# Kernel optimization log

Hardware: AMD Instinct MI355X
Metric: run time of the kernel (lower is better)

The kernel has to match this reference:

```python
import jax, jax.numpy as jnp
import numpy as np

N = 50000      # nodes
E = 800000     # edges (avg degree 16)
NFEAT = 256
NHID = 128
NCLASS = 40
NLAYERS_MID = 13  # gc2..gc14


def setup_inputs() -> dict:
    key = jax.random.key(0)
    ks = jax.random.split(key, 16)
    stdv_h = 1.0 / np.sqrt(NHID)     # GraphConvolution stdv = 1/sqrt(out_features)
    stdv_c = 1.0 / np.sqrt(NCLASS)
    u = lambda k, shape, s: jax.random.uniform(k, shape, jnp.float32, -s, s)
    return {
        "x": jax.random.normal(ks[0], (N, NFEAT), jnp.float32),
        "edge_src": jax.random.randint(ks[1], (E,), 0, N, jnp.int32),
        "edge_dst": jax.random.randint(ks[2], (E,), 0, N, jnp.int32),
        "edge_weight": jax.random.uniform(ks[3], (E,), jnp.float32),
        # skip-branch linear (self.weight / self.bias)
        "W0": u(ks[4], (NFEAT, NHID), stdv_h),
        "b0": u(ks[5], (NHID,), stdv_h),
        # gc1: nfeat -> nhid
        "W1": u(ks[6], (NFEAT, NHID), stdv_h),
        "b1": u(ks[7], (NHID,), stdv_h),
        # gc2..gc14: nhid -> nhid, stacked
        "Wmid": u(ks[8], (NLAYERS_MID, NHID, NHID), stdv_h),
        "bmid": u(ks[9], (NLAYERS_MID, NHID), stdv_h),
        # gc15: 14*nhid -> nclass
        "W15": u(ks[10], (14 * NHID, NCLASS), stdv_c),
        "b15": u(ks[11], (NCLASS,), stdv_c),
    }


def reference(x, edge_src, edge_dst, edge_weight, W0, b0, W1, b1, Wmid, bmid, W15, b15):
    n = x.shape[0]

    def gcn(h, W, b):
        # support = h @ W ; out = spmm(adj, support) + b  (adj as weighted edge list)
        support = h @ W
        msgs = support[edge_src] * edge_weight[:, None]           # [E, d]
        agg = jax.ops.segment_sum(msgs, edge_dst, num_segments=n)  # [N, d]
        return agg + b

    z = x @ W0 + b0
    x1 = jax.nn.relu(gcn(x, W1, b1)) + z

    def step(h, Wb):
        W, b = Wb
        hn = jax.nn.relu(gcn(h, W, b)) + h
        return hn, hn

    _, xs = jax.lax.scan(step, x1, (Wmid, bmid))   # xs: [13, N, NHID] = x2..x14
    all_x = jnp.concatenate([x1[None], xs], axis=0)  # [14, N, NHID] = x1..x14
    # concat order in torch code: (x14, x13, ..., x1)
    x_cat = jnp.swapaxes(all_x[::-1], 0, 1).reshape(n, 14 * NHID)
    # dropout is identity in eval mode
    x15 = gcn(x_cat, W15, b15)
    return jax.nn.log_softmax(x15, axis=1)
```

## Files before the change

kernel.cpp:

```cpp
#include <hip/hip_runtime.h>
#include <stdint.h>

#define NN 50000
#define EE 800000
#define DH 128
#define NC 40
#define KCAT (14*DH)
#define CAP 64

typedef __bf16 bf16x8 __attribute__((ext_vector_type(8)));
typedef float floatx4 __attribute__((ext_vector_type(4)));

__device__ __forceinline__ float bf2f(unsigned short u) {
  union { uint32_t i; float f; } v; v.i = ((uint32_t)u) << 16; return v.f;
}
__device__ __forceinline__ unsigned short f2bf(float f) {
  union { float f; uint32_t i; } v; v.f = f;
  uint32_t x = v.i;
  uint32_t r = (x + 0x7fffu + ((x >> 16) & 1u)) >> 16;
  return (unsigned short)r;
}

__global__ void init_counts_detect(int* counts, const unsigned short* xw) {
  int i = blockIdx.x * blockDim.x + threadIdx.x;
  if (i < NN) counts[i] = 0;
  if (blockIdx.x == 0) {
    int t = threadIdx.x;
    int wild = 0;
    for (int k = t; k < 4096; k += 256) {
      unsigned e = (xw[k] >> 7) & 0xFF;
      if (e >= 0x90) wild++;
    }
    __shared__ int red[256];
    red[t] = wild;
    __syncthreads();
    for (int s = 128; s > 0; s >>= 1) {
      if (t < s) red[t] += red[t + s];
      __syncthreads();
    }
    if (t == 0) counts[NN] = red[0];
  }
}

__global__ void convert_f4(const void* in, unsigned short* outp, int n4, const int* flag) {
  bool isf32 = (*flag) > 32;
  for (int i = blockIdx.x * blockDim.x + threadIdx.x; i < n4;
       i += gridDim.x * blockDim.x) {
    ushort4 o;
    if (isf32) {
      float4 v = ((const float4*)in)[i];
      o.x = f2bf(v.x); o.y = f2bf(v.y); o.z = f2bf(v.z); o.w = f2bf(v.w);
    } else {
      o = ((const ushort4*)in)[i];
    }
    ((ushort4*)outp)[i] = o;
  }
}

__global__ void convert_bias(const void* b0, const void* b1, const void* bm,
                             const void* b15, unsigned short* bb, const int* flag) {
  bool isf32 = (*flag) > 32;
  int i = blockIdx.x * blockDim.x + threadIdx.x;
  if (i >= 1960) return;
  const void* src; int off;
  if (i < 128)        { src = b0;  off = i; }
  else if (i < 256)   { src = b1;  off = i - 128; }
  else if (i < 1920)  { src = bm;  off = i - 256; }
  else                { src = b15; off = i - 1920; }
  bb[i] = isf32 ? f2bf(((const float*)src)[off]) : ((const unsigned short*)src)[off];
}

__global__ void transpose_w(const void* B, unsigned short* BT,
                            int L, int K, int M, int Mpad, const int* flag) {
  bool isf32 = (*flag) > 32;
  int total = L * Mpad * K;
  for (int idx = blockIdx.x * blockDim.x + threadIdx.x; idx < total;
       idx += gridDim.x * blockDim.x) {
    int k = idx % K;
    int n = (idx / K) % Mpad;
    int l = idx / (K * Mpad);
    unsigned short v = 0;
    if (n < M) {
      size_t si = (size_t)l * K * M + (size_t)k * M + n;
      v = isf32 ? f2bf(((const float*)B)[si]) : ((const unsigned short*)B)[si];
    }
    BT[idx] = v;
  }
}

__global__ void build_ell(const int* __restrict__ src, const int* __restrict__ dst,
                          const void* __restrict__ w,
                          int* __restrict__ cnt, int2* __restrict__ ell,
                          const int* __restrict__ flag) {
  bool isf32 = (*flag) > 32;
  int e = blockIdx.x * blockDim.x + threadIdx.x;
  if (e >= EE) return;
  int d = dst[e];
  if ((unsigned)d >= NN) return;
  int p = atomicAdd(&cnt[d], 1);
  if (p >= CAP) return;
  int s = src[e];
  float wf = isf32 ? ((const float*)w)[e] : bf2f(((const unsigned short*)w)[e]);
  if ((unsigned)s >= NN) { s = 0; wf = 0.f; }
  union { float f; int i; } wv; wv.f = wf;
  ell[(size_t)d * CAP + p] = make_int2(s, wv.i);
}

template <int K>
__global__ __launch_bounds__(256) void gemm_direct(
    const unsigned short* __restrict__ A, int lda,
    const unsigned short* __restrict__ BT,
    unsigned short* __restrict__ C, int ldc,
    const unsigned short* __restrict__ bias) {
  int t = threadIdx.x;
  int wave = t >> 6, lane = t & 63;
  int q = lane >> 4, mn = lane & 15;
  int r0 = blockIdx.x * 64;
  int wcol = wave * 32;

  const unsigned short* ap[4];
  #pragma unroll
  for (int i = 0; i < 4; ++i) {
    int r = r0 + i * 16 + mn;
    if (r >= NN) r = NN - 1;
    ap[i] = A + (size_t)r * lda + q * 8;
  }
  const unsigned short* bp[2];
  #pragma unroll
  for (int j = 0; j < 2; ++j) bp[j] = BT + (size_t)(wcol + j * 16 + mn) * K + q * 8;

  floatx4 acc[4][2];
  floatx4 zf = {0.f, 0.f, 0.f, 0.f};
  #pragma unroll
  for (int i = 0; i < 4; ++i)
    #pragma unroll
    for (int j = 0; j < 2; ++j) acc[i][j] = zf;

  #pragma unroll
  for (int kc = 0; kc < K; kc += 64) {
    bf16x8 fa[4][2], fb[2][2];
    #pragma unroll
    for (int i = 0; i < 4; ++i)
      #pragma unroll
      for (int ks = 0; ks < 2; ++ks)
        fa[i][ks] = *(const bf16x8*)(ap[i] + kc + ks * 32);
    #pragma unroll
    for (int j = 0; j < 2; ++j)
      #pragma unroll
      for (int ks = 0; ks < 2; ++ks)
        fb[j][ks] = *(const bf16x8*)(bp[j] + kc + ks * 32);
    #pragma unroll
    for (int ks = 0; ks < 2; ++ks)
      #pragma unroll
      for (int i = 0; i < 4; ++i)
        #pragma unroll
        for (int j = 0; j < 2; ++j)
          acc[i][j] = __builtin_amdgcn_mfma_f32_16x16x32_bf16(fa[i][ks], fb[j][ks],
                                                              acc[i][j], 0, 0, 0);
  }

  #pragma unroll
  for (int j = 0; j < 2; ++j) {
    int col = wcol + j * 16 + mn;
    float badd = bias ? bf2f(bias[col]) : 0.0f;
    #pragma unroll
    for (int i = 0; i < 4; ++i) {
      int rbase = r0 + i * 16 + q * 4;
      #pragma unroll
      for (int rr = 0; rr < 4; ++rr) {
        int row = rbase + rr;
        if (row < NN) C[(size_t)row * ldc + col] = f2bf(acc[i][j][rr] + badd);
      }
    }
  }
}

__global__ __launch_bounds__(256) void gemm_cat_direct(
    const unsigned short* __restrict__ A,
    const unsigned short* __restrict__ BT,
    float* __restrict__ C) {
  int t = threadIdx.x;
  int wave = t >> 6, lane = t & 63;
  int q = lane >> 4, mn = lane & 15;
  int r0 = blockIdx.x * 64 + wave * 16;
  int ar = r0 + mn;
  if (ar >= NN) ar = NN - 1;
  const unsigned short* ap = A + (size_t)ar * KCAT + q * 8;
  const unsigned short* bp[3];
  #pragma unroll
  for (int j = 0; j < 3; ++j) bp[j] = BT + (size_t)(j * 16 + mn) * KCAT + q * 8;

  floatx4 acc[3];
  floatx4 zf = {0.f, 0.f, 0.f, 0.f};
  #pragma unroll
  for (int j = 0; j < 3; ++j) acc[j] = zf;

  #pragma unroll 2
  for (int kc = 0; kc < KCAT; kc += 64) {
    bf16x8 fa[2], fb[3][2];
    #pragma unroll
    for (int ks = 0; ks < 2; ++ks) fa[ks] = *(const bf16x8*)(ap + kc + ks * 32);
    #pragma unroll
    for (int j = 0; j < 3; ++j)
      #pragma unroll
      for (int ks = 0; ks < 2; ++ks)
        fb[j][ks] = *(const bf16x8*)(bp[j] + kc + ks * 32);
    #pragma unroll
    for (int ks = 0; ks < 2; ++ks)
      #pragma unroll
      for (int j = 0; j < 3; ++j)
        acc[j] = __builtin_amdgcn_mfma_f32_16x16x32_bf16(fa[ks], fb[j][ks], acc[j],
                                                         0, 0, 0);
  }

  #pragma unroll
  for (int j = 0; j < 3; ++j) {
    int col = j * 16 + mn;
    if (col < NC) {
      #pragma unroll
      for (int rr = 0; rr < 4; ++rr) {
        int row = r0 + q * 4 + rr;
        if (row < NN) C[(size_t)row * NC + col] = acc[j][rr];
      }
    }
  }
}

__global__ __launch_bounds__(256) void spmm_layer(
    const unsigned short* __restrict__ support, const int* __restrict__ cnt,
    const int2* __restrict__ ell, const unsigned short* __restrict__ bias,
    const unsigned short* __restrict__ res, int res_stride,
    unsigned short* __restrict__ out, int out_stride) {
  int wave = threadIdx.x >> 6, lane = threadIdx.x & 63;
  int row = blockIdx.x * 4 + wave;
  if (row >= NN) return;
  int n = cnt[row];
  if (n > CAP) n = CAP;
  int2 ev = ell[(size_t)row * CAP + lane];
  float a0 = 0.f, a1 = 0.f;
  int j = 0;
  for (; j + 16 <= n; j += 16) {
    uint32_t g[16];
    int sidx[16];
    #pragma unroll
    for (int u = 0; u < 16; ++u) sidx[u] = __shfl(ev.x, j + u);
    #pragma unroll
    for (int u = 0; u < 16; ++u)
      g[u] = *(const uint32_t*)(support + (size_t)sidx[u] * DH + 2 * lane);
    #pragma unroll
    for (int u = 0; u < 16; ++u) {
      union { int i; float f; } wv; wv.i = __shfl(ev.y, j + u);
      a0 += wv.f * bf2f((unsigned short)(g[u] & 0xffff));
      a1 += wv.f * bf2f((unsigned short)(g[u] >> 16));
    }
  }
  for (; j + 8 <= n; j += 8) {
    uint32_t g[8];
    int sidx[8];
    #pragma unroll
    for (int u = 0; u < 8; ++u) sidx[u] = __shfl(ev.x, j + u);
    #pragma unroll
    for (int u = 0; u < 8; ++u)
      g[u] = *(const uint32_t*)(support + (size_t)sidx[u] * DH + 2 * lane);
    #pragma unroll
    for (int u = 0; u < 8; ++u) {
      union { int i; float f; } wv; wv.i = __shfl(ev.y, j + u);
      a0 += wv.f * bf2f((unsigned short)(g[u] & 0xffff));
      a1 += wv.f * bf2f((unsigned short)(g[u] >> 16));
    }
  }
  for (; j < n; ++j) {
    int s = __shfl(ev.x, j);
    union { int i; float f; } wv; wv.i = __shfl(ev.y, j);
    uint32_t g = *(const uint32_t*)(support + (size_t)s * DH + 2 * lane);
    a0 += wv.f * bf2f((unsigned short)(g & 0xffff));
    a1 += wv.f * bf2f((unsigned short)(g >> 16));
  }
  uint32_t bw = *(const uint32_t*)(bias + 2 * lane);
  uint32_t rw = *(const uint32_t*)(res + (size_t)row * res_stride + 2 * lane);
  float v0 = fmaxf(a0 + bf2f((unsigned short)(bw & 0xffff)), 0.f) +
             bf2f((unsigned short)(rw & 0xffff));
  float v1 = fmaxf(a1 + bf2f((unsigned short)(bw >> 16)), 0.f) +
             bf2f((unsigned short)(rw >> 16));
  uint32_t o = (uint32_t)f2bf(v0) | ((uint32_t)f2bf(v1) << 16);
  *(uint32_t*)(out + (size_t)row * out_stride + 2 * lane) = o;
}

__global__ __launch_bounds__(256) void spmm_softmax_out(
    const float* __restrict__ s15, const int* __restrict__ cnt,
    const int2* __restrict__ ell, const unsigned short* __restrict__ bias,
    float* __restrict__ out) {
  int wave = threadIdx.x >> 6, lane = threadIdx.x & 63;
  int row = blockIdx.x * 4 + wave;
  if (row >= NN) return;
  int n = cnt[row];
  if (n > CAP) n = CAP;
  int2 ev = ell[(size_t)row * CAP + lane];
  int fl = lane < NC ? lane : NC - 1;
  float acc = 0.f;
  int j = 0;
  for (; j + 4 <= n; j += 4) {
    float g[4];
    #pragma unroll
    for (int u = 0; u < 4; ++u) {
      int s = __shfl(ev.x, j + u);
      g[u] = s15[(size_t)s * NC + fl];
    }
    #pragma unroll
    for (int u = 0; u < 4; ++u) {
      union { int i; float f; } wv; wv.i = __shfl(ev.y, j + u);
      acc += wv.f * g[u];
    }
  }
  for (; j < n; ++j) {
    int s = __shfl(ev.x, j);
    union { int i; float f; } wv; wv.i = __shfl(ev.y, j);
    acc += wv.f * s15[(size_t)s * NC + fl];
  }
  acc += bf2f(bias[fl]);
  float v = (lane < NC) ? acc : -3.0e38f;
  float m = v;
  #pragma unroll
  for (int off = 32; off > 0; off >>= 1) m = fmaxf(m, __shfl_xor(m, off));
  float e = (lane < NC) ? expf(v - m) : 0.f;
  float sum = e;
  #pragma unroll
  for (int off = 32; off > 0; off >>= 1) sum += __shfl_xor(sum, off);
  if (lane < NC) out[(size_t)row * NC + lane] = v - m - logf(sum);
}

extern "C" void kernel_launch(void* const* d_in, const int* in_sizes, int n_in,
                              void* d_out, int out_size, void* d_ws, size_t ws_size,
                              hipStream_t stream) {
  const void* x   = d_in[0];
  const int* esrc = (const int*)d_in[1];
  const int* edst = (const int*)d_in[2];
  const void* ew  = d_in[3];
  const void* W0  = d_in[4];
  const void* b0  = d_in[5];
  const void* W1  = d_in[6];
  const void* b1  = d_in[7];
  const void* Wm  = d_in[8];
  const void* bm  = d_in[9];
  const void* W15 = d_in[10];
  const void* b15 = d_in[11];
  float* out = (float*)d_out;

  char* ws = (char*)d_ws;
  size_t off = 0;
  auto alloc = [&](size_t bytes) -> void* {
    void* p = ws + off;
    off = (off + bytes + 255) & ~(size_t)255;
    return p;
  };
  unsigned short* xcat = (unsigned short*)alloc((size_t)NN * KCAT * 2);
  unsigned short* xbf  = (unsigned short*)alloc((size_t)NN * 256 * 2);
  unsigned short* supp = (unsigned short*)alloc((size_t)NN * DH * 2);
  unsigned short* zbuf = (unsigned short*)alloc((size_t)NN * DH * 2);
  float* s15           = (float*)alloc((size_t)NN * NC * 4);
  int* counts          = (int*)alloc((size_t)(NN + 1) * 4);
  int2* ell            = (int2*)alloc((size_t)NN * CAP * 8);
  unsigned short* W0T  = (unsigned short*)alloc((size_t)256 * 128 * 2);
  unsigned short* W1T  = (unsigned short*)alloc((size_t)256 * 128 * 2);
  unsigned short* WmT  = (unsigned short*)alloc((size_t)13 * 128 * 128 * 2);
  unsigned short* W15T = (unsigned short*)alloc((size_t)48 * 1792 * 2);
  unsigned short* bb   = (unsigned short*)alloc((size_t)(128 + 128 + 13 * 128 + 40) * 2);
  if (off > ws_size) return;
  int* flag = counts + NN;
  unsigned short* b0b  = bb;
  unsigned short* b1b  = bb + 128;
  unsigned short* bmb  = bb + 256;
  unsigned short* b15b = bb + 256 + 13 * 128;

  init_counts_detect<<<197, 256, 0, stream>>>(counts, (const unsigned short*)x);
  transpose_w<<<128, 256, 0, stream>>>(W0, W0T, 1, 256, 128, 128, flag);
  transpose_w<<<128, 256, 0, stream>>>(W1, W1T, 1, 256, 128, 128, flag);
  transpose_w<<<832, 256, 0, stream>>>(Wm, WmT, 13, 128, 128, 128, flag);
  transpose_w<<<336, 256, 0, stream>>>(W15, W15T, 1, 1792, 40, 48, flag);
  convert_f4<<<2048, 256, 0, stream>>>(x, xbf, NN * 256 / 4, flag);
  convert_bias<<<8, 256, 0, stream>>>(b0, b1, bm, b15, bb, flag);
  build_ell<<<3125, 256, 0, stream>>>(esrc, edst, ew, counts, ell, flag);

  int gb = (NN + 63) / 64;
  int sb = (NN + 3) / 4;
  gemm_direct<256><<<gb, 256, 0, stream>>>(xbf, 256, W0T, zbuf, DH, b0b);
  gemm_direct<256><<<gb, 256, 0, stream>>>(xbf, 256, W1T, supp, DH, nullptr);
  spmm_layer<<<sb, 256, 0, stream>>>(supp, counts, ell, b1b, zbuf, DH,
                                     xcat + 13 * DH, KCAT);
  for (int l = 0; l < 13; ++l) {
    gemm_direct<128><<<gb, 256, 0, stream>>>(xcat + (13 - l) * DH, KCAT,
                                             WmT + l * 128 * 128, supp, DH, nullptr);
    spmm_layer<<<sb, 256, 0, stream>>>(supp, counts, ell, bmb + l * DH,
                                       xcat + (13 - l) * DH, KCAT,
                                       xcat + (12 - l) * DH, KCAT);
  }
  gemm_cat_direct<<<gb, 256, 0, stream>>>(xcat, W15T, s15);
  spmm_softmax_out<<<sb, 256, 0, stream>>>(s15, counts, ell, b15b, out);
}
```

Baseline: 1.093 ms.

## Stage GEMM A tiles in LDS via direct global-to-LDS loads and fuse first GEMMs

After: 1.017 ms. 6.9% less time.

```diff
diff --git a/kernel.cpp b/kernel.cpp
--- a/kernel.cpp
+++ b/kernel.cpp
@@ -10,6 +10,11 @@
 
 typedef __bf16 bf16x8 __attribute__((ext_vector_type(8)));
 typedef float floatx4 __attribute__((ext_vector_type(4)));
+
+#define GLOAD_LDS16(gp, lp)                                                          \
+  __builtin_amdgcn_global_load_lds(                                                  \
+      (const __attribute__((address_space(1))) uint32_t*)(gp),                       \
+      (__attribute__((address_space(3))) uint32_t*)(lp), 16, 0, 0)
 
 __device__ __forceinline__ float bf2f(unsigned short u) {
   union { uint32_t i; float f; } v; v.i = ((uint32_t)u) << 16; return v.f;
@@ -106,111 +111,183 @@
   ell[(size_t)d * CAP + p] = make_int2(s, wv.i);
 }
 
-template <int K>
-__global__ __launch_bounds__(256) void gemm_direct(
-    const unsigned short* __restrict__ A, int lda,
+__global__ __launch_bounds__(256) void gemm_first(
+    const unsigned short* __restrict__ A,
     const unsigned short* __restrict__ BT,
-    unsigned short* __restrict__ C, int ldc,
+    unsigned short* __restrict__ C0,
+    unsigned short* __restrict__ C1,
     const unsigned short* __restrict__ bias) {
+  __shared__ unsigned short As[64 * 256];
   int t = threadIdx.x;
   int wave = t >> 6, lane = t & 63;
   int q = lane >> 4, mn = lane & 15;
   int r0 = blockIdx.x * 64;
-  int wcol = wave * 32;
-
-  const unsigned short* ap[4];
-  #pragma unroll
-  for (int i = 0; i < 4; ++i) {
-    int r = r0 + i * 16 + mn;
-    if (r >= NN) r = NN - 1;
-    ap[i] = A + (size_t)r * lda + q * 8;
-  }
-  const unsigned short* bp[2];
-  #pragma unroll
-  for (int j = 0; j < 2; ++j) bp[j] = BT + (size_t)(wcol + j * 16 + mn) * K + q * 8;
-
-  floatx4 acc[4][2];
+
+  #pragma unroll
+  for (int cc = 0; cc < 8; ++cc) {
+    int L = cc * 4096 + t * 16;
+    int row = L >> 9;
+    int colb = (L & 511) ^ ((row & 7) << 4);
+    int gr = r0 + row; if (gr >= NN) gr = NN - 1;
+    GLOAD_LDS16((const char*)A + (size_t)gr * 512 + colb, (char*)As + L);
+  }
+  __syncthreads();
+
+  floatx4 acc[4][4];
   floatx4 zf = {0.f, 0.f, 0.f, 0.f};
   #pragma unroll
   for (int i = 0; i < 4; ++i)
     #pragma unroll
-    for (int j = 0; j < 2; ++j) acc[i][j] = zf;
-
-  #pragma unroll
-  for (int kc = 0; kc < K; kc += 64) {
-    bf16x8 fa[4][2], fb[2][2];
+    for (int j = 0; j < 4; ++j) acc[i][j] = zf;
+
+  #pragma unroll
+  for (int ks = 0; ks < 8; ++ks) {
+    bf16x8 fa[4], fb[4];
+    #pragma unroll
+    for (int i = 0; i < 4; ++i) {
+      int row = i * 16 + mn;
+      fa[i] = *(const bf16x8*)((const char*)As + row * 512 +
+                               ((ks * 64 + q * 16) ^ ((row & 7) << 4)));
+    }
+    #pragma unroll
+    for (int j = 0; j < 4; ++j)
+      fb[j] = *(const bf16x8*)((const char*)BT +
+                               (size_t)(wave * 64 + j * 16 + mn) * 512 + ks * 64 + q * 16);
     #pragma unroll
     for (int i = 0; i < 4; ++i)
       #pragma unroll
-      for (int ks = 0; ks < 2; ++ks)
-        fa[i][ks] = *(const bf16x8*)(ap[i] + kc + ks * 32);
-    #pragma unroll
-    for (int j = 0; j < 2; ++j)
-      #pragma unroll
-      for (int ks = 0; ks < 2; ++ks)
-        fb[j][ks] = *(const bf16x8*)(bp[j] + kc + ks * 32);
-    #pragma unroll
-    for (int ks = 0; ks < 2; ++ks)
-      #pragma unroll
-      for (int i = 0; i < 4; ++i)
-        #pragma unroll
-        for (int j = 0; j < 2; ++j)
-          acc[i][j] = __builtin_amdgcn_mfma_f32_16x16x32_bf16(fa[i][ks], fb[j][ks],
-                                                              acc[i][j], 0, 0, 0);
-  }
-
-  #pragma unroll
-  for (int j = 0; j < 2; ++j) {
-    int col = wcol + j * 16 + mn;
-    float badd = bias ? bf2f(bias[col]) : 0.0f;
+      for (int j = 0; j < 4; ++j)
+        acc[i][j] = __builtin_amdgcn_mfma_f32_16x16x32_bf16(fa[i], fb[j], acc[i][j], 0, 0, 0);
+  }
+
+  #pragma unroll
+  for (int j = 0; j < 4; ++j) {
+    int col = wave * 64 + j * 16 + mn;
+    bool is0 = col < 128;
+    int ccol = is0 ? col : col - 128;
+    unsigned short* Cp = is0 ? C0 : C1;
+    float badd = is0 ? bf2f(bias[ccol]) : 0.f;
     #pragma unroll
     for (int i = 0; i < 4; ++i) {
       int rbase = r0 + i * 16 + q * 4;
       #pragma unroll
       for (int rr = 0; rr < 4; ++rr) {
         int row = rbase + rr;
-        if (row < NN) C[(size_t)row * ldc + col] = f2bf(acc[i][j][rr] + badd);
+        if (row < NN) Cp[(size_t)row * 128 + ccol] = f2bf(acc[i][j][rr] + badd);
       }
     }
   }
 }
 
-__global__ __launch_bounds__(256) void gemm_cat_direct(
+__global__ __launch_bounds__(256) void gemm_mid(
+    const unsigned short* __restrict__ A,
+    const unsigned short* __restrict__ BT,
+    unsigned short* __restrict__ C) {
+  __shared__ unsigned short As[32 * 128];
+  int t = threadIdx.x;
+  int wave = t >> 6, lane = t & 63;
+  int q = lane >> 4, mn = lane & 15;
+  int r0 = blockIdx.x * 32;
+
+  #pragma unroll
+  for (int cc = 0; cc < 2; ++cc) {
+    int L = cc * 4096 + t * 16;
+    int row = L >> 8;
+    int colb = (L & 255) ^ ((row & 7) << 4);
+    int gr = r0 + row; if (gr >= NN) gr = NN - 1;
+    GLOAD_LDS16((const char*)A + (size_t)gr * (KCAT * 2) + colb, (char*)As + L);
+  }
+  __syncthreads();
+
+  floatx4 acc[2][2];
+  floatx4 zf = {0.f, 0.f, 0.f, 0.f};
+  #pragma unroll
+  for (int i = 0; i < 2; ++i)
+    #pragma unroll
+    for (int j = 0; j < 2; ++j) acc[i][j] = zf;
+
+  #pragma unroll
+  for (int ks = 0; ks < 4; ++ks) {
+    bf16x8 fa[2], fb[2];
+    #pragma unroll
+    for (int i = 0; i < 2; ++i) {
+      int row = i * 16 + mn;
+      fa[i] = *(const bf16x8*)((const char*)As + row * 256 +
+                               ((ks * 64 + q * 16) ^ ((row & 7) << 4)));
+    }
+    #pragma unroll
+    for (int j = 0; j < 2; ++j)
+      fb[j] = *(const bf16x8*)((const char*)BT +
+                               (size_t)(wave * 32 + j * 16 + mn) * 256 + ks * 64 + q * 16);
+    #pragma unroll
+    for (int i = 0; i < 2; ++i)
+      #pragma unroll
+      for (int j = 0; j < 2; ++j)
+        acc[i][j] = __builtin_amdgcn_mfma_f32_16x16x32_bf16(fa[i], fb[j], acc[i][j], 0, 0, 0);
+  }
+
+  #pragma unroll
+  for (int i = 0; i < 2; ++i) {
+    int rbase = r0 + i * 16 + q * 4;
+    #pragma unroll
+    for (int j = 0; j < 2; ++j) {
+      int col = wave * 32 + j * 16 + mn;
+      #pragma unroll
+      for (int rr = 0; rr < 4; ++rr) {
+        int row = rbase + rr;
+        if (row < NN) C[(size_t)row * 128 + col] = f2bf(acc[i][j][rr]);
+      }
+    }
+  }
+}
+
+__global__ __launch_bounds__(256) void gemm_cat2(
     const unsigned short* __restrict__ A,
     const unsigned short* __restrict__ BT,
     float* __restrict__ C) {
+  __shared__ unsigned short As[2][64 * 128];
   int t = threadIdx.x;
   int wave = t >> 6, lane = t & 63;
   int q = lane >> 4, mn = lane & 15;
-  int r0 = blockIdx.x * 64 + wave * 16;
-  int ar = r0 + mn;
-  if (ar >= NN) ar = NN - 1;
-  const unsigned short* ap = A + (size_t)ar * KCAT + q * 8;
-  const unsigned short* bp[3];
-  #pragma unroll
-  for (int j = 0; j < 3; ++j) bp[j] = BT + (size_t)(j * 16 + mn) * KCAT + q * 8;
+  int r0 = blockIdx.x * 64;
 
   floatx4 acc[3];
   floatx4 zf = {0.f, 0.f, 0.f, 0.f};
   #pragma unroll
   for (int j = 0; j < 3; ++j) acc[j] = zf;
 
-  #pragma unroll 2
-  for (int kc = 0; kc < KCAT; kc += 64) {
-    bf16x8 fa[2], fb[3][2];
-    #pragma unroll
-    for (int ks = 0; ks < 2; ++ks) fa[ks] = *(const bf16x8*)(ap + kc + ks * 32);
-    #pragma unroll
-    for (int j = 0; j < 3; ++j)
-      #pragma unroll
-      for (int ks = 0; ks < 2; ++ks)
-        fb[j][ks] = *(const bf16x8*)(bp[j] + kc + ks * 32);
-    #pragma unroll
-    for (int ks = 0; ks < 2; ++ks)
+  auto stage = [&](int c) {
+    #pragma unroll
+    for (int cc = 0; cc < 4; ++cc) {
+      int L = cc * 4096 + t * 16;
+      int row = L >> 8;
+      int colb = (L & 255) ^ ((row & 7) << 4);
+      int gr = r0 + row; if (gr >= NN) gr = NN - 1;
+      GLOAD_LDS16((const char*)A + (size_t)gr * 3584 + c * 256 + colb,
+                  (char*)As[c & 1] + L);
+    }
+  };
+
+  stage(0);
+  __syncthreads();
+  for (int c = 0; c < 14; ++c) {
+    if (c + 1 < 14) stage(c + 1);
+    const char* buf = (const char*)As[c & 1];
+    int rloc = wave * 16 + mn;
+    int rsw = (rloc & 7) << 4;
+    #pragma unroll
+    for (int ks = 0; ks < 4; ++ks) {
+      bf16x8 fa = *(const bf16x8*)(buf + rloc * 256 + ((ks * 64 + q * 16) ^ rsw));
+      bf16x8 fb[3];
       #pragma unroll
       for (int j = 0; j < 3; ++j)
-        acc[j] = __builtin_amdgcn_mfma_f32_16x16x32_bf16(fa[ks], fb[j][ks], acc[j],
-                                                         0, 0, 0);
+        fb[j] = *(const bf16x8*)((const char*)BT + (size_t)(j * 16 + mn) * 3584 +
+                                 c * 256 + ks * 64 + q * 16);
+      #pragma unroll
+      for (int j = 0; j < 3; ++j)
+        acc[j] = __builtin_amdgcn_mfma_f32_16x16x32_bf16(fa, fb[j], acc[j], 0, 0, 0);
+    }
+    if (c + 1 < 14) __syncthreads();
   }
 
   #pragma unroll
@@ -219,7 +296,7 @@
     if (col < NC) {
       #pragma unroll
       for (int rr = 0; rr < 4; ++rr) {
-        int row = r0 + q * 4 + rr;
+        int row = r0 + wave * 16 + q * 4 + rr;
         if (row < NN) C[(size_t)row * NC + col] = acc[j][rr];
       }
     }
@@ -360,8 +437,7 @@
   float* s15           = (float*)alloc((size_t)NN * NC * 4);
   int* counts          = (int*)alloc((size_t)(NN + 1) * 4);
   int2* ell            = (int2*)alloc((size_t)NN * CAP * 8);
-  unsigned short* W0T  = (unsigned short*)alloc((size_t)256 * 128 * 2);
-  unsigned short* W1T  = (unsigned short*)alloc((size_t)256 * 128 * 2);
+  unsigned short* W01T = (unsigned short*)alloc((size_t)256 * 256 * 2);
   unsigned short* WmT  = (unsigned short*)alloc((size_t)13 * 128 * 128 * 2);
   unsigned short* W15T = (unsigned short*)alloc((size_t)48 * 1792 * 2);
   unsigned short* bb   = (unsigned short*)alloc((size_t)(128 + 128 + 13 * 128 + 40) * 2);
@@ -373,27 +449,27 @@
   unsigned short* b15b = bb + 256 + 13 * 128;
 
   init_counts_detect<<<197, 256, 0, stream>>>(counts, (const unsigned short*)x);
-  transpose_w<<<128, 256, 0, stream>>>(W0, W0T, 1, 256, 128, 128, flag);
-  transpose_w<<<128, 256, 0, stream>>>(W1, W1T, 1, 256, 128, 128, flag);
+  transpose_w<<<128, 256, 0, stream>>>(W0, W01T, 1, 256, 128, 128, flag);
+  transpose_w<<<128, 256, 0, stream>>>(W1, W01T + 128 * 256, 1, 256, 128, 128, flag);
   transpose_w<<<832, 256, 0, stream>>>(Wm, WmT, 13, 128, 128, 128, flag);
   transpose_w<<<336, 256, 0, stream>>>(W15, W15T, 1, 1792, 40, 48, flag);
   convert_f4<<<2048, 256, 0, stream>>>(x, xbf, NN * 256 / 4, flag);
   convert_bias<<<8, 256, 0, stream>>>(b0, b1, bm, b15, bb, flag);
   build_ell<<<3125, 256, 0, stream>>>(esrc, edst, ew, counts, ell, flag);
 
-  int gb = (NN + 63) / 64;
-  int sb = (NN + 3) / 4;
-  gemm_direct<256><<<gb, 256, 0, stream>>>(xbf, 256, W0T, zbuf, DH, b0b);
-  gemm_direct<256><<<gb, 256, 0, stream>>>(xbf, 256, W1T, supp, DH, nullptr);
+  int gb64 = (NN + 63) / 64;
+  int gb32 = (NN + 31) / 32;
+  int sb   = (NN + 3) / 4;
+  gemm_first<<<gb64, 256, 0, stream>>>(xbf, W01T, zbuf, supp, b0b);
   spmm_layer<<<sb, 256, 0, stream>>>(supp, counts, ell, b1b, zbuf, DH,
                                      xcat + 13 * DH, KCAT);
   for (int l = 0; l < 13; ++l) {
-    gemm_direct<128><<<gb, 256, 0, stream>>>(xcat + (13 - l) * DH, KCAT,
-                                             WmT + l * 128 * 128, supp, DH, nullptr);
+    gemm_mid<<<gb32, 256, 0, stream>>>(xcat + (13 - l) * DH,
+                                       WmT + l * 128 * 128, supp);
     spmm_layer<<<sb, 256, 0, stream>>>(supp, counts, ell, bmb + l * DH,
                                        xcat + (13 - l) * DH, KCAT,
                                        xcat + (12 - l) * DH, KCAT);
   }
-  gemm_cat_direct<<<gb, 256, 0, stream>>>(xcat, W15T, s15);
+  gemm_cat2<<<gb64, 256, 0, stream>>>(xcat, W15T, s15);
   spmm_softmax_out<<<sb, 256, 0, stream>>>(s15, counts, ell, b15b, out);
 }
```
